# Optimization experiments

Hardware: AMD Instinct MI355X
Metric: run time of the kernel (lower is better)

The kernel has to match this reference:

```python
import jax, jax.numpy as jnp
import numpy as np

LN_EPS = 1e-5

def setup_inputs() -> dict:
    num_nodes, embed_dim, bs, E = 10000, 64, 32, 200000
    key = jax.random.key(0)
    ks = jax.random.split(key, 8)
    d_in = 2 * embed_dim + 1  # msg_dim = 1
    d_h = 4 * embed_dim
    return {
        "users": jax.random.randint(ks[0], (E,), 0, num_nodes * bs),
        "items": jax.random.randint(ks[1], (E,), 0, num_nodes * bs),
        "messages": jax.random.normal(ks[2], (E,), dtype=jnp.float32),
        "bs": bs,
        "user_emb": jax.random.normal(ks[3], (num_nodes, embed_dim), dtype=jnp.float32) * 0.02,
        "item_emb": jax.random.normal(ks[4], (num_nodes, embed_dim), dtype=jnp.float32) * 0.02,
        "W1": jax.random.normal(ks[5], (d_in, d_h), dtype=jnp.float32) * 0.02,
        "b1": jnp.zeros((d_h,), dtype=jnp.float32),
        "ln_g": jnp.ones((d_h,), dtype=jnp.float32),
        "ln_b": jnp.zeros((d_h,), dtype=jnp.float32),
        "W2": jax.random.normal(ks[6], (d_h, d_h), dtype=jnp.float32) * 0.02,
        "b2": jnp.zeros((d_h,), dtype=jnp.float32),
    }

def reference(users, items, messages, bs, user_emb, item_emb, W1, b1, ln_g, ln_b, W2, b2):
    num_nodes, embed_dim = user_emb.shape
    N = num_nodes * bs
    msgs = messages.astype(jnp.float32).reshape(-1, 1)          # [E,1]
    ue = user_emb[users % num_nodes]                             # [E,D]
    ie = item_emb[items % num_nodes]                             # [E,D]
    x = jnp.concatenate([ue, ie, msgs], axis=-1)                 # [E,2D+1]
    h = x @ W1 + b1                                              # [E,4D]
    mu = jnp.mean(h, axis=-1, keepdims=True)
    var = jnp.mean(jnp.square(h - mu), axis=-1, keepdims=True)
    hn = (h - mu) * jax.lax.rsqrt(var + LN_EPS) * ln_g + ln_b
    enc = hn @ W2 + b2                                           # [E,4D]
    uu, iu, ug, ig = jnp.split(enc, 4, axis=-1)                  # each [E,D]
    user_state = jnp.zeros((N, embed_dim), jnp.float32).at[users].add(uu)
    item_state = jnp.zeros((N, embed_dim), jnp.float32).at[items].add(iu)
    user_global = jnp.zeros((N, embed_dim), jnp.float32).at[users].add(ug)
    item_global = jnp.zeros((N, embed_dim), jnp.float32).at[items].add(ig)
    # reshape (num_nodes, bs, D) -> (bs, num_nodes, D)
    up = jnp.transpose(user_global.reshape(num_nodes, bs, embed_dim), (1, 0, 2))
    ip = jnp.transpose(item_global.reshape(num_nodes, bs, embed_dim), (1, 0, 2))
    up = jnp.mean(up, axis=1, keepdims=True)                     # [bs,1,D]
    ip = jnp.mean(ip, axis=1, keepdims=True)
    ret_u = jnp.transpose(user_state.reshape(num_nodes, bs, embed_dim), (1, 0, 2)) + up
    ret_i = jnp.transpose(item_state.reshape(num_nodes, bs, embed_dim), (1, 0, 2)) + ip
    return (ret_u, ret_i)
```

## Files before the change

### kernel.cpp

```cpp
#include <hip/hip_runtime.h>
#include <hip/hip_bf16.h>


typedef __attribute__((ext_vector_type(8))) short bf8_t;
typedef __attribute__((ext_vector_type(4))) float f32x4;

union FragU { bf8_t f; unsigned int u[4]; };

static __device__ __forceinline__ unsigned short f2bf(float f) {
    unsigned int x = __float_as_uint(f);
    return (unsigned short)((x + 0x7fffu + ((x >> 16) & 1u)) >> 16);
}
#define B2F_LO(u) __uint_as_float((u) << 16)
#define B2F_HI(u) __uint_as_float((u) & 0xffff0000u)

__global__ void zero_f4_kernel(float4* p, int n4) {
    int i = blockIdx.x * 256 + threadIdx.x;
    int stride = gridDim.x * 256;
    float4 z = make_float4(0.f, 0.f, 0.f, 0.f);
    for (; i < n4; i += stride) p[i] = z;
}

__global__ void convert_kernel(const float* __restrict__ W1, const float* __restrict__ W2,
                               const float* __restrict__ uemb, const float* __restrict__ iemb,
                               unsigned short* __restrict__ w1f, unsigned short* __restrict__ w2f,
                               unsigned short* __restrict__ uembb, unsigned short* __restrict__ iembb,
                               int nemb4) {
    int idx = blockIdx.x * 256 + threadIdx.x;
    if (idx < 4096) {
        int l = idx & 63, fr = idx >> 6;
        int ks = fr & 3, nt = fr >> 2;
        int n = nt * 16 + (l & 15), g = l >> 4;
        unsigned short v[8];
#pragma unroll
        for (int e = 0; e < 8; e++) {
            int k = ks * 32 + ((e < 4) ? (4 * g + e) : (16 + 4 * g + (e - 4)));
            v[e] = f2bf(W1[k * 256 + n]);
        }
        uint4 pk;
        pk.x = (unsigned)v[0] | ((unsigned)v[1] << 16);
        pk.y = (unsigned)v[2] | ((unsigned)v[3] << 16);
        pk.z = (unsigned)v[4] | ((unsigned)v[5] << 16);
        pk.w = (unsigned)v[6] | ((unsigned)v[7] << 16);
        *(uint4*)&w1f[idx * 8] = pk;
    } else if (idx < 12288) {
        int t = idx - 4096;
        int l = t & 63, fr = t >> 6;
        int ks = fr & 7, nt = fr >> 3;
        int n = nt * 16 + (l & 15), g = l >> 4;
        unsigned short v[8];
#pragma unroll
        for (int e = 0; e < 8; e++) {
            int k = ks * 32 + ((e < 4) ? (4 * g + e) : (16 + 4 * g + (e - 4)));
            v[e] = f2bf(W2[k * 256 + n]);
        }
        uint4 pk;
        pk.x = (unsigned)v[0] | ((unsigned)v[1] << 16);
        pk.y = (unsigned)v[2] | ((unsigned)v[3] << 16);
        pk.z = (unsigned)v[4] | ((unsigned)v[5] << 16);
        pk.w = (unsigned)v[6] | ((unsigned)v[7] << 16);
        *(uint4*)&w2f[t * 8] = pk;
    }
    if (nemb4 > 0) {
        int total = gridDim.x * 256;
        for (int i = idx; i < 2 * nemb4; i += total) {
            int isU = (i < nemb4);
            int j = isU ? i : i - nemb4;
            float4 v = isU ? ((const float4*)uemb)[j] : ((const float4*)iemb)[j];
            ushort4 p;
            p.x = f2bf(v.x); p.y = f2bf(v.y); p.z = f2bf(v.z); p.w = f2bf(v.w);
            unsigned short* dst = isU ? uembb : iembb;
            *(ushort4*)&dst[(long)j * 4] = p;
        }
    }
}

__global__ __launch_bounds__(512, 2)
void encode_mfma_kernel(const int* __restrict__ users, const int* __restrict__ items,
                        const float* __restrict__ msgs,
                        const float* __restrict__ uemb, const float* __restrict__ iemb,
                        const unsigned short* __restrict__ uembb, const unsigned short* __restrict__ iembb,
                        const float* __restrict__ W1, const float* __restrict__ b1,
                        const float* __restrict__ ln_g, const float* __restrict__ ln_b,
                        const float* __restrict__ b2,
                        const unsigned short* __restrict__ w1f, const unsigned short* __restrict__ w2f,
                        float* __restrict__ out, float* __restrict__ glob,
                        int E, int num_nodes, int bs, long out_half, int usebf) {
    __shared__ __align__(16) unsigned short xhb[64 * 256];
    __shared__ __align__(16) float gacc[4096];
    __shared__ __align__(16) float msgs_s[64];
    __shared__ __align__(16) int ubase_s[64], ibase_s[64];

    const int tid = threadIdx.x;
    const int w = tid >> 6;
    const int l = tid & 63;
    const int g = l >> 4;
    const int m16 = l & 15;
    const int nnD = num_nodes * 64;

    for (int i = tid; i < 4096; i += 512) gacc[i] = 0.f;

    bf8_t w1frag[2][4], w2frag[2][8];
#pragma unroll
    for (int ntl = 0; ntl < 2; ntl++) {
        int nt = w * 2 + ntl;
#pragma unroll
        for (int ks = 0; ks < 4; ks++)
            w1frag[ntl][ks] = *(const bf8_t*)&w1f[((nt * 4 + ks) * 64 + l) * 8];
#pragma unroll
        for (int ks = 0; ks < 8; ks++)
            w2frag[ntl][ks] = *(const bf8_t*)&w2f[((nt * 8 + ks) * 64 + l) * 8];
    }

    float b1v[2], w128v[2], b2v[2];
#pragma unroll
    for (int ntl = 0; ntl < 2; ntl++) {
        int j = w * 32 + ntl * 16 + m16;
        b1v[ntl] = b1[j];
        w128v[ntl] = W1[128 * 256 + j];
        b2v[ntl] = b2[j];
    }
    float* outi = out + out_half;

    const int nTiles = (E + 63) >> 6;
    for (int tile = blockIdx.x; tile < nTiles; tile += gridDim.x) {
        const int e0 = tile << 6;
        __syncthreads();

        if (tid < 64) {
            int ev = e0 + tid;
            if (ev < E) {
                int u = users[ev], it = items[ev];
                int ub = u % bs, un = u / bs, ib = it % bs, in_ = it / bs;
                ubase_s[tid] = (ub * nnD + un * 64) | (ub << 26);
                ibase_s[tid] = (ib * nnD + in_ * 64) | (ib << 26);
                msgs_s[tid] = msgs[ev];
            } else {
                ubase_s[tid] = -1; ibase_s[tid] = -1; msgs_s[tid] = 0.f;
            }
        }
        for (int idx = tid; idx < 1024; idx += 512) {
            int e = idx >> 4, q = idx & 15;
            int ev = e0 + e;
            uint4 v = make_uint4(0u, 0u, 0u, 0u);
            if (ev < E) {
                if (usebf) {
                    if (q < 8) { int u = users[ev] % num_nodes; v = *(const uint4*)&uembb[(long)u * 64 + q * 8]; }
                    else       { int it = items[ev] % num_nodes; v = *(const uint4*)&iembb[(long)it * 64 + (q - 8) * 8]; }
                } else {
                    const float* src; long base;
                    if (q < 8) { int u = users[ev] % num_nodes; src = uemb; base = (long)u * 64 + q * 8; }
                    else       { int it = items[ev] % num_nodes; src = iemb; base = (long)it * 64 + (q - 8) * 8; }
                    float4 a0 = *(const float4*)&src[base];
                    float4 a1 = *(const float4*)&src[base + 4];
                    v.x = (unsigned)f2bf(a0.x) | ((unsigned)f2bf(a0.y) << 16);
                    v.y = (unsigned)f2bf(a0.z) | ((unsigned)f2bf(a0.w) << 16);
                    v.z = (unsigned)f2bf(a1.x) | ((unsigned)f2bf(a1.y) << 16);
                    v.w = (unsigned)f2bf(a1.z) | ((unsigned)f2bf(a1.w) << 16);
                }
            }
            int byte = (q * 16) ^ ((e & 7) << 4);
            *(uint4*)&xhb[e * 128 + (byte >> 1)] = v;
        }
        __syncthreads();

        f32x4 acc[4][2];
#pragma unroll
        for (int mt = 0; mt < 4; mt++) {
            const float* mgp = &msgs_s[mt * 16 + 4 * g];
            float mg[4] = {mgp[0], mgp[1], mgp[2], mgp[3]};
#pragma unroll
            for (int ntl = 0; ntl < 2; ntl++) {
                f32x4 a;
#pragma unroll
                for (int r = 0; r < 4; r++) a[r] = fmaf(mg[r], w128v[ntl], b1v[ntl]);
                acc[mt][ntl] = a;
            }
        }
#pragma unroll
        for (int ks = 0; ks < 4; ks++) {
            FragU a[4];
#pragma unroll
            for (int mt = 0; mt < 4; mt++) {
                int i = mt * 16 + m16;
                int bir0 = (ks * 64 + 8 * g) ^ ((i & 7) << 4);
                int bir1 = (ks * 64 + 32 + 8 * g) ^ ((i & 7) << 4);
                uint2 c0 = *(const uint2*)&xhb[i * 128 + (bir0 >> 1)];
                uint2 c1 = *(const uint2*)&xhb[i * 128 + (bir1 >> 1)];
                a[mt].u[0] = c0.x; a[mt].u[1] = c0.y; a[mt].u[2] = c1.x; a[mt].u[3] = c1.y;
            }
#pragma unroll
            for (int ntl = 0; ntl < 2; ntl++)
#pragma unroll
                for (int mt = 0; mt < 4; mt++)
                    acc[mt][ntl] = __builtin_amdgcn_mfma_f32_16x16x32_bf16(
                        a[mt].f, w1frag[ntl][ks], acc[mt][ntl], 0, 0, 0);
        }
        __syncthreads();

#pragma unroll
        for (int mt = 0; mt < 4; mt++)
#pragma unroll
            for (int ntl = 0; ntl < 2; ntl++)
#pragma unroll
                for (int r = 0; r < 4; r++) {
                    int e = mt * 16 + 4 * g + r;
                    int j = w * 32 + ntl * 16 + m16;
                    int byte = (2 * j) ^ ((e & 15) << 4);
                    xhb[e * 256 + (byte >> 1)] = f2bf(acc[mt][ntl][r]);
                }
        __syncthreads();

#pragma unroll
        for (int it = 0; it < 4; it++) {
            int e = w * 8 + it * 2 + (l >> 5);
            int slot = l & 31;
            int byte = (slot * 16) ^ ((e & 15) << 4);
            uint4 hv = *(const uint4*)&xhb[e * 256 + (byte >> 1)];
            float f0 = B2F_LO(hv.x), f1 = B2F_HI(hv.x);
            float f2 = B2F_LO(hv.y), f3 = B2F_HI(hv.y);
            float f4 = B2F_LO(hv.z), f5 = B2F_HI(hv.z);
            float f6 = B2F_LO(hv.w), f7 = B2F_HI(hv.w);
            float s1 = ((f0 + f1) + (f2 + f3)) + ((f4 + f5) + (f6 + f7));
            float s2 = ((f0*f0 + f1*f1) + (f2*f2 + f3*f3)) + ((f4*f4 + f5*f5) + (f6*f6 + f7*f7));
#pragma unroll
            for (int mk = 1; mk <= 16; mk <<= 1) {
                s1 += __shfl_xor(s1, mk);
                s2 += __shfl_xor(s2, mk);
            }
            float mu = s1 * (1.f / 256.f);
            float var = s2 * (1.f / 256.f) - mu * mu;
            float rs = rsqrtf(var + 1e-5f);
            int jb = (slot ^ (e & 15)) * 8;
            float4 g0 = *(const float4*)&ln_g[jb];
            float4 g1 = *(const float4*)&ln_g[jb + 4];
            float4 bb0 = *(const float4*)&ln_b[jb];
            float4 bb1 = *(const float4*)&ln_b[jb + 4];
            float n0 = fmaf((f0 - mu) * rs, g0.x, bb0.x);
            float n1 = fmaf((f1 - mu) * rs, g0.y, bb0.y);
            float n2 = fmaf((f2 - mu) * rs, g0.z, bb0.z);
            float n3 = fmaf((f3 - mu) * rs, g0.w, bb0.w);
            float n4 = fmaf((f4 - mu) * rs, g1.x, bb1.x);
            float n5 = fmaf((f5 - mu) * rs, g1.y, bb1.y);
            float n6 = fmaf((f6 - mu) * rs, g1.z, bb1.z);
            float n7 = fmaf((f7 - mu) * rs, g1.w, bb1.w);
            uint4 pv;
            pv.x = (unsigned)f2bf(n0) | ((unsigned)f2bf(n1) << 16);
            pv.y = (unsigned)f2bf(n2) | ((unsigned)f2bf(n3) << 16);
            pv.z = (unsigned)f2bf(n4) | ((unsigned)f2bf(n5) << 16);
            pv.w = (unsigned)f2bf(n6) | ((unsigned)f2bf(n7) << 16);
            *(uint4*)&xhb[e * 256 + (byte >> 1)] = pv;
        }
        __syncthreads();

#pragma unroll
        for (int mt = 0; mt < 4; mt++)
#pragma unroll
            for (int ntl = 0; ntl < 2; ntl++) {
                f32x4 a;
#pragma unroll
                for (int r = 0; r < 4; r++) a[r] = b2v[ntl];
                acc[mt][ntl] = a;
            }
#pragma unroll
        for (int ks = 0; ks < 8; ks++) {
            FragU a[4];
#pragma unroll
            for (int mt = 0; mt < 4; mt++) {
                int i = mt * 16 + m16;
                int bir0 = (ks * 64 + 8 * g) ^ ((i & 15) << 4);
                int bir1 = (ks * 64 + 32 + 8 * g) ^ ((i & 15) << 4);
                uint2 c0 = *(const uint2*)&xhb[i * 256 + (bir0 >> 1)];
                uint2 c1 = *(const uint2*)&xhb[i * 256 + (bir1 >> 1)];
                a[mt].u[0] = c0.x; a[mt].u[1] = c0.y; a[mt].u[2] = c1.x; a[mt].u[3] = c1.y;
            }
#pragma unroll
            for (int ntl = 0; ntl < 2; ntl++)
#pragma unroll
                for (int mt = 0; mt < 4; mt++)
                    acc[mt][ntl] = __builtin_amdgcn_mfma_f32_16x16x32_bf16(
                        a[mt].f, w2frag[ntl][ks], acc[mt][ntl], 0, 0, 0);
        }

        const int q = w >> 1;
        const int dbase = (w & 1) * 32;
        const int* barr = (q & 1) ? ibase_s : ubase_s;
#pragma unroll
        for (int mt = 0; mt < 4; mt++) {
            int4 bb = *(const int4*)&barr[mt * 16 + 4 * g];
            int bvv[4] = {bb.x, bb.y, bb.z, bb.w};
#pragma unroll
            for (int ntl = 0; ntl < 2; ntl++) {
                int d = dbase + ntl * 16 + m16;
#pragma unroll
                for (int r = 0; r < 4; r++) {
                    int v = bvv[r];
                    if (v >= 0) {
                        float val = acc[mt][ntl][r];
                        if (q == 0)      atomicAdd(&out[(v & 0x03FFFFFF) + d], val);
                        else if (q == 1) atomicAdd(&outi[(v & 0x03FFFFFF) + d], val);
                        else if (q == 2) atomicAdd(&gacc[(v >> 26) * 64 + d], val);
                        else             atomicAdd(&gacc[2048 + (v >> 26) * 64 + d], val);
                    }
                }
            }
        }
    }

    __syncthreads();
    for (int i = tid; i < 4096; i += 512) {
        float v = gacc[i];
        if (v != 0.f) atomicAdd(&glob[i], v);
    }
}

__global__ void finalize_kernel(float* __restrict__ out, const float* __restrict__ glob,
                                long out_half, long nnD, float inv_nodes, int n4) {
    int i4 = blockIdx.x * 256 + threadIdx.x;
    int stride = gridDim.x * 256;
    for (; i4 < n4; i4 += stride) {
        long i = (long)i4 * 4;
        int half = (i >= out_half) ? 1 : 0;
        long r = half ? (i - out_half) : i;
        int b = (int)(r / nnD);
        int dq = (int)(i & 63);
        float4 gv = *(const float4*)&glob[half * 2048 + b * 64 + dq];
        float4 o = ((float4*)out)[i4];
        o.x += gv.x * inv_nodes;
        o.y += gv.y * inv_nodes;
        o.z += gv.z * inv_nodes;
        o.w += gv.w * inv_nodes;
        ((float4*)out)[i4] = o;
    }
}

extern "C" void kernel_launch(void* const* d_in, const int* in_sizes, int n_in,
                              void* d_out, int out_size, void* d_ws, size_t ws_size,
                              hipStream_t stream) {
    const int* users = (const int*)d_in[0];
    const int* items = (const int*)d_in[1];
    const float* msgs = (const float*)d_in[2];
    const float* uemb = (const float*)d_in[4];
    const float* iemb = (const float*)d_in[5];
    const float* W1 = (const float*)d_in[6];
    const float* b1 = (const float*)d_in[7];
    const float* ln_g = (const float*)d_in[8];
    const float* ln_b = (const float*)d_in[9];
    const float* W2 = (const float*)d_in[10];
    const float* b2 = (const float*)d_in[11];

    const int E = in_sizes[0];
    const int dh = in_sizes[7];
    const int D = dh / 4;
    const int num_nodes = in_sizes[4] / D;
    const long out_half = (long)out_size / 2;
    const int bs = (int)(out_half / ((long)num_nodes * D));

    float* out = (float*)d_out;
    float* glob = (float*)d_ws;
    unsigned short* w1f = (unsigned short*)((char*)d_ws + 16384);
    unsigned short* w2f = (unsigned short*)((char*)d_ws + 16384 + 65536);
    size_t embb_off = 16384 + 65536 + 131072;
    size_t embb_bytes = (size_t)num_nodes * 64 * 2;
    int usebf = (ws_size >= embb_off + 2 * embb_bytes) ? 1 : 0;
    unsigned short* uembb = usebf ? (unsigned short*)((char*)d_ws + embb_off) : nullptr;
    unsigned short* iembb = usebf ? (unsigned short*)((char*)d_ws + embb_off + embb_bytes) : nullptr;
    int nemb4 = usebf ? (num_nodes * 16) : 0;

    zero_f4_kernel<<<2048, 256, 0, stream>>>((float4*)out, out_size / 4);
    zero_f4_kernel<<<4, 256, 0, stream>>>((float4*)glob, 4096 / 4);
    convert_kernel<<<256, 256, 0, stream>>>(W1, W2, uemb, iemb, w1f, w2f, uembb, iembb, nemb4);

    encode_mfma_kernel<<<256, 512, 0, stream>>>(
        users, items, msgs, uemb, iemb, uembb, iembb,
        W1, b1, ln_g, ln_b, b2, w1f, w2f, out, glob,
        E, num_nodes, bs, out_half, usebf);

    finalize_kernel<<<2048, 256, 0, stream>>>(out, glob, out_half,
                                              (long)num_nodes * 64, 1.0f / num_nodes,
                                              out_size / 4);
}
```

Baseline: 471.6 us.

## Prefetch next tile's indices and embeddings, stream weight fragments, raise occupancy

The embedding gather for the next tile is software-pipelined. Indices are loaded after the first barrier and embedding rows are fetched into registers during the LayerNorm/second-GEMM phase, so global latency overlaps compute. The W1/W2 MFMA fragments are no longer held in registers for the whole kernel. They are reloaded per k-step from global/L2, which frees VGPRs so launch bounds can go from 2 to 4 blocks per CU and the grid from 256 to 512 blocks. The usebf branch becomes a template parameter. The risks are extra repeated weight loads per tile and possible register spills under the tighter bound.

```diff
diff --git a/kernel.cpp b/kernel.cpp
--- a/kernel.cpp
+++ b/kernel.cpp
@@ -75,7 +75,8 @@
     }
 }
 
-__global__ __launch_bounds__(512, 2)
+template<bool USEBF>
+__global__ __launch_bounds__(512, 4)
 void encode_mfma_kernel(const int* __restrict__ users, const int* __restrict__ items,
                         const float* __restrict__ msgs,
                         const float* __restrict__ uemb, const float* __restrict__ iemb,
@@ -85,7 +86,7 @@
                         const float* __restrict__ b2,
                         const unsigned short* __restrict__ w1f, const unsigned short* __restrict__ w2f,
                         float* __restrict__ out, float* __restrict__ glob,
-                        int E, int num_nodes, int bs, long out_half, int usebf) {
+                        int E, int num_nodes, int bs, long out_half) {
     __shared__ __align__(16) unsigned short xhb[64 * 256];
     __shared__ __align__(16) float gacc[4096];
     __shared__ __align__(16) float msgs_s[64];
@@ -100,18 +101,6 @@
 
     for (int i = tid; i < 4096; i += 512) gacc[i] = 0.f;
 
-    bf8_t w1frag[2][4], w2frag[2][8];
-#pragma unroll
-    for (int ntl = 0; ntl < 2; ntl++) {
-        int nt = w * 2 + ntl;
-#pragma unroll
-        for (int ks = 0; ks < 4; ks++)
-            w1frag[ntl][ks] = *(const bf8_t*)&w1f[((nt * 4 + ks) * 64 + l) * 8];
-#pragma unroll
-        for (int ks = 0; ks < 8; ks++)
-            w2frag[ntl][ks] = *(const bf8_t*)&w2f[((nt * 8 + ks) * 64 + l) * 8];
-    }
-
     float b1v[2], w128v[2], b2v[2];
 #pragma unroll
     for (int ntl = 0; ntl < 2; ntl++) {
@@ -122,47 +111,74 @@
     }
     float* outi = out + out_half;
 
+    const int ce = tid >> 4;
+    const int cq = tid & 15;
+    int praw[2];
+    int pu = -1, pi = -1; float pmsg = 0.f;
+    uint4 pemb[2];
+
     const int nTiles = (E + 63) >> 6;
-    for (int tile = blockIdx.x; tile < nTiles; tile += gridDim.x) {
-        const int e0 = tile << 6;
+    const int tstep = gridDim.x;
+
+    auto prefetch_idx = [&](int e0p) {
+#pragma unroll
+        for (int c = 0; c < 2; c++) {
+            int ev = e0p + ce + 32 * c;
+            praw[c] = (ev < E) ? ((cq < 8) ? users[ev] : items[ev]) : 0;
+        }
+        if (tid < 64) {
+            int ev = e0p + tid;
+            if (ev < E) { pu = users[ev]; pi = items[ev]; pmsg = msgs[ev]; }
+            else        { pu = -1; pi = -1; pmsg = 0.f; }
+        }
+    };
+    auto prefetch_emb = [&]() {
+#pragma unroll
+        for (int c = 0; c < 2; c++) {
+            int row = praw[c] % num_nodes;
+            if (USEBF) {
+                const unsigned short* t = (cq < 8) ? uembb : iembb;
+                pemb[c] = *(const uint4*)&t[(long)row * 64 + (cq & 7) * 8];
+            } else {
+                const float* tf = (cq < 8) ? uemb : iemb;
+                long base = (long)row * 64 + (cq & 7) * 8;
+                float4 a0 = *(const float4*)&tf[base];
+                float4 a1 = *(const float4*)&tf[base + 4];
+                pemb[c].x = (unsigned)f2bf(a0.x) | ((unsigned)f2bf(a0.y) << 16);
+                pemb[c].y = (unsigned)f2bf(a0.z) | ((unsigned)f2bf(a0.w) << 16);
+                pemb[c].z = (unsigned)f2bf(a1.x) | ((unsigned)f2bf(a1.y) << 16);
+                pemb[c].w = (unsigned)f2bf(a1.z) | ((unsigned)f2bf(a1.w) << 16);
+            }
+        }
+    };
+
+    if (blockIdx.x < nTiles) {
+        prefetch_idx(blockIdx.x << 6);
+        prefetch_emb();
+    }
+
+    for (int tile = blockIdx.x; tile < nTiles; tile += tstep) {
         __syncthreads();
 
         if (tid < 64) {
-            int ev = e0 + tid;
-            if (ev < E) {
-                int u = users[ev], it = items[ev];
-                int ub = u % bs, un = u / bs, ib = it % bs, in_ = it / bs;
+            if (pu >= 0) {
+                int ub = pu % bs, un = pu / bs, ib = pi % bs, in_ = pi / bs;
                 ubase_s[tid] = (ub * nnD + un * 64) | (ub << 26);
                 ibase_s[tid] = (ib * nnD + in_ * 64) | (ib << 26);
-                msgs_s[tid] = msgs[ev];
+                msgs_s[tid] = pmsg;
             } else {
                 ubase_s[tid] = -1; ibase_s[tid] = -1; msgs_s[tid] = 0.f;
             }
         }
-        for (int idx = tid; idx < 1024; idx += 512) {
-            int e = idx >> 4, q = idx & 15;
-            int ev = e0 + e;
-            uint4 v = make_uint4(0u, 0u, 0u, 0u);
-            if (ev < E) {
-                if (usebf) {
-                    if (q < 8) { int u = users[ev] % num_nodes; v = *(const uint4*)&uembb[(long)u * 64 + q * 8]; }
-                    else       { int it = items[ev] % num_nodes; v = *(const uint4*)&iembb[(long)it * 64 + (q - 8) * 8]; }
-                } else {
-                    const float* src; long base;
-                    if (q < 8) { int u = users[ev] % num_nodes; src = uemb; base = (long)u * 64 + q * 8; }
-                    else       { int it = items[ev] % num_nodes; src = iemb; base = (long)it * 64 + (q - 8) * 8; }
-                    float4 a0 = *(const float4*)&src[base];
-                    float4 a1 = *(const float4*)&src[base + 4];
-                    v.x = (unsigned)f2bf(a0.x) | ((unsigned)f2bf(a0.y) << 16);
-                    v.y = (unsigned)f2bf(a0.z) | ((unsigned)f2bf(a0.w) << 16);
-                    v.z = (unsigned)f2bf(a1.x) | ((unsigned)f2bf(a1.y) << 16);
-                    v.w = (unsigned)f2bf(a1.z) | ((unsigned)f2bf(a1.w) << 16);
-                }
-            }
-            int byte = (q * 16) ^ ((e & 7) << 4);
-            *(uint4*)&xhb[e * 128 + (byte >> 1)] = v;
+#pragma unroll
+        for (int c = 0; c < 2; c++) {
+            int e = ce + 32 * c;
+            int byte = (cq * 16) ^ ((e & 7) << 4);
+            *(uint4*)&xhb[e * 128 + (byte >> 1)] = pemb[c];
         }
         __syncthreads();
+
+        prefetch_idx((tile + tstep) << 6);
 
         f32x4 acc[4][2];
 #pragma unroll
@@ -179,6 +195,8 @@
         }
 #pragma unroll
         for (int ks = 0; ks < 4; ks++) {
+            bf8_t wf0 = *(const bf8_t*)&w1f[(((w * 2 + 0) * 4 + ks) * 64 + l) * 8];
+            bf8_t wf1 = *(const bf8_t*)&w1f[(((w * 2 + 1) * 4 + ks) * 64 + l) * 8];
             FragU a[4];
 #pragma unroll
             for (int mt = 0; mt < 4; mt++) {
@@ -190,11 +208,11 @@
                 a[mt].u[0] = c0.x; a[mt].u[1] = c0.y; a[mt].u[2] = c1.x; a[mt].u[3] = c1.y;
             }
 #pragma unroll
-            for (int ntl = 0; ntl < 2; ntl++)
-#pragma unroll
-                for (int mt = 0; mt < 4; mt++)
-                    acc[mt][ntl] = __builtin_amdgcn_mfma_f32_16x16x32_bf16(
-                        a[mt].f, w1frag[ntl][ks], acc[mt][ntl], 0, 0, 0);
+            for (int mt = 0; mt < 4; mt++)
+                acc[mt][0] = __builtin_amdgcn_mfma_f32_16x16x32_bf16(a[mt].f, wf0, acc[mt][0], 0, 0, 0);
+#pragma unroll
+            for (int mt = 0; mt < 4; mt++)
+                acc[mt][1] = __builtin_amdgcn_mfma_f32_16x16x32_bf16(a[mt].f, wf1, acc[mt][1], 0, 0, 0);
         }
         __syncthreads();
 
@@ -210,6 +228,8 @@
                     xhb[e * 256 + (byte >> 1)] = f2bf(acc[mt][ntl][r]);
                 }
         __syncthreads();
+
+        prefetch_emb();
 
 #pragma unroll
         for (int it = 0; it < 4; it++) {
@@ -264,6 +284,8 @@
             }
 #pragma unroll
         for (int ks = 0; ks < 8; ks++) {
+            bf8_t wf0 = *(const bf8_t*)&w2f[(((w * 2 + 0) * 8 + ks) * 64 + l) * 8];
+            bf8_t wf1 = *(const bf8_t*)&w2f[(((w * 2 + 1) * 8 + ks) * 64 + l) * 8];
             FragU a[4];
 #pragma unroll
             for (int mt = 0; mt < 4; mt++) {
@@ -275,11 +297,11 @@
                 a[mt].u[0] = c0.x; a[mt].u[1] = c0.y; a[mt].u[2] = c1.x; a[mt].u[3] = c1.y;
             }
 #pragma unroll
-            for (int ntl = 0; ntl < 2; ntl++)
-#pragma unroll
-                for (int mt = 0; mt < 4; mt++)
-                    acc[mt][ntl] = __builtin_amdgcn_mfma_f32_16x16x32_bf16(
-                        a[mt].f, w2frag[ntl][ks], acc[mt][ntl], 0, 0, 0);
+            for (int mt = 0; mt < 4; mt++)
+                acc[mt][0] = __builtin_amdgcn_mfma_f32_16x16x32_bf16(a[mt].f, wf0, acc[mt][0], 0, 0, 0);
+#pragma unroll
+            for (int mt = 0; mt < 4; mt++)
+                acc[mt][1] = __builtin_amdgcn_mfma_f32_16x16x32_bf16(a[mt].f, wf1, acc[mt][1], 0, 0, 0);
         }
 
         const int q = w >> 1;
@@ -371,10 +393,16 @@
     zero_f4_kernel<<<4, 256, 0, stream>>>((float4*)glob, 4096 / 4);
     convert_kernel<<<256, 256, 0, stream>>>(W1, W2, uemb, iemb, w1f, w2f, uembb, iembb, nemb4);
 
-    encode_mfma_kernel<<<256, 512, 0, stream>>>(
-        users, items, msgs, uemb, iemb, uembb, iembb,
-        W1, b1, ln_g, ln_b, b2, w1f, w2f, out, glob,
-        E, num_nodes, bs, out_half, usebf);
+    if (usebf)
+        encode_mfma_kernel<true><<<512, 512, 0, stream>>>(
+            users, items, msgs, uemb, iemb, uembb, iembb,
+            W1, b1, ln_g, ln_b, b2, w1f, w2f, out, glob,
+            E, num_nodes, bs, out_half);
+    else
+        encode_mfma_kernel<false><<<512, 512, 0, stream>>>(
+            users, items, msgs, uemb, iemb, uembb, iembb,
+            W1, b1, ln_g, ln_b, b2, w1f, w2f, out, glob,
+            E, num_nodes, bs, out_half);
 
     finalize_kernel<<<2048, 256, 0, stream>>>(out, glob, out_half,
                                               (long)num_nodes * 64, 1.0f / num_nodes,
```

After: 622.1 us. +31.9%, slower.
